# Kernel tuning notes

Measured on AMD Instinct MI355X. Metric: run time of the kernel, lower is better.

Reference implementation:

```python
import jax, jax.numpy as jnp
import numpy as np

B, S, D, H = 2, 4096, 512, 8
DK = D // H  # 64


def setup_inputs() -> dict:
    key = jax.random.key(0)
    ks = jax.random.split(key, 7)
    scale = 1.0 / np.sqrt(D)
    return {
        "query": jax.random.normal(ks[0], (B, S, D), dtype=jnp.float32),
        "key": jax.random.normal(ks[1], (B, S, D), dtype=jnp.float32),
        "value": jax.random.normal(ks[2], (B, S, D), dtype=jnp.float32),
        # nn.Linear weights, stored [out, in] as in torch; y = x @ W.T
        "Wq": jax.random.normal(ks[3], (D, D), dtype=jnp.float32) * scale,
        "Wk": jax.random.normal(ks[4], (D, D), dtype=jnp.float32) * scale,
        "Wv": jax.random.normal(ks[5], (D, D), dtype=jnp.float32) * scale,
        "Wo": jax.random.normal(ks[6], (D, D), dtype=jnp.float32) * scale,
    }


def reference(query, key, value, Wq, Wk, Wv, Wo):
    # projections (torch Linear: x @ W.T)
    q = query @ Wq.T  # [B,S,D]
    k = key @ Wk.T
    v = value @ Wv.T
    # split heads -> [B,H,S,DK]
    q = q.reshape(B, S, H, DK).transpose(0, 2, 1, 3)
    k = k.reshape(B, S, H, DK).transpose(0, 2, 1, 3)
    v = v.reshape(B, S, H, DK).transpose(0, 2, 1, 3)
    # scores [B,H,S,S], softmax, weighted sum (dropout=0 / eval)
    scores = jnp.einsum("bhqd,bhkd->bhqk", q, k) / np.sqrt(DK).astype(np.float32)
    weights = jax.nn.softmax(scores, axis=-1)
    attn = jnp.einsum("bhqk,bhkd->bhqd", weights, v)  # [B,H,S,DK]
    # merge heads -> [B,S,D], output projection
    out = attn.transpose(0, 2, 1, 3).reshape(B, S, D)
    return out @ Wo.T
```

## Files before the change

### kernel.cpp

```cpp
#include <hip/hip_runtime.h>
#include <hip/hip_bf16.h>

typedef short short8 __attribute__((ext_vector_type(8)));
typedef short short4v __attribute__((ext_vector_type(4)));
typedef float floatx4 __attribute__((ext_vector_type(4)));
typedef unsigned int uint4v __attribute__((ext_vector_type(4)));

constexpr int Bc = 2, Sc = 4096, Dc = 512, Hc = 8, DKc = 64;
constexpr int Mc = Bc * Sc;

static __device__ __forceinline__ unsigned short f2bf(float f) {
  unsigned int u = __builtin_bit_cast(unsigned int, f);
  unsigned int rb = ((u >> 16) & 1u) + 0x7fffu;
  return (unsigned short)((u + rb) >> 16);
}
static __device__ __forceinline__ unsigned int cvt_pk_bf16(float lo, float hi) {
  unsigned int r;
  asm("v_cvt_pk_bf16_f32 %0, %1, %2" : "=v"(r) : "v"(lo), "v"(hi));
  return r;
}
static __device__ __forceinline__ float exp2_fast(float x) {
  float r;
  asm("v_exp_f32 %0, %1" : "=v"(r) : "v"(x));
  return r;
}

__global__ __launch_bounds__(256) void cast_w(
    const float* __restrict__ a, const float* __restrict__ b,
    const float* __restrict__ c, const float* __restrict__ d,
    unsigned short* __restrict__ out) {
  const float* srcs[4] = {a, b, c, d};
  const int m = blockIdx.y;
  const int i = (blockIdx.x * 256 + threadIdx.x) * 4;
  float4 v = *(const float4*)(srcs[m] + i);
  unsigned short t4[4] = {f2bf(v.x), f2bf(v.y), f2bf(v.z), f2bf(v.w)};
  *(short4v*)(out + (size_t)m * (Dc * Dc) + i) = *(short4v*)t4;
}

template <int IN_F32, int OUT_F32>
__global__ __launch_bounds__(256) void gemm_bt(
    const void* __restrict__ Xv, const unsigned short* __restrict__ Wb,
    void* __restrict__ Yv, int Mdim, int N, int K) {
  constexpr int BM = 128, BN = 64, BK = 32, LDP = 40;
  __shared__ unsigned short As[BM * LDP];
  __shared__ unsigned short Bs[BN * LDP];
  const int tid = threadIdx.x;
  const int lane = tid & 63, wid = tid >> 6;
  const int wm = wid >> 1, wn = wid & 1;
  const int bm = blockIdx.y * BM, bn = blockIdx.x * BN;
  const int rq = lane & 15, kk8 = (lane >> 4) * 8;
  const int sr = tid >> 1, sc = (tid & 1) * 16;
  const int brow = tid >> 2, bc8 = (tid & 3) * 8;

  floatx4 acc[4][2] = {};

  for (int k0 = 0; k0 < K; k0 += BK) {
    if (IN_F32) {
      const float* src = (const float*)Xv + (size_t)(bm + sr) * K + k0 + sc;
      unsigned int t2[8];
#pragma unroll
      for (int i = 0; i < 4; ++i) {
        float4 v = *(const float4*)(src + i * 4);
        t2[i * 2 + 0] = cvt_pk_bf16(v.x, v.y);
        t2[i * 2 + 1] = cvt_pk_bf16(v.z, v.w);
      }
      uint4v u0 = {t2[0], t2[1], t2[2], t2[3]};
      uint4v u1 = {t2[4], t2[5], t2[6], t2[7]};
      *(uint4v*)&As[sr * LDP + sc] = u0;
      *(uint4v*)&As[sr * LDP + sc + 8] = u1;
    } else {
      const unsigned short* src =
          (const unsigned short*)Xv + (size_t)(bm + sr) * K + k0 + sc;
      *(short8*)&As[sr * LDP + sc] = *(const short8*)src;
      *(short8*)&As[sr * LDP + sc + 8] = *(const short8*)(src + 8);
    }
    *(short8*)&Bs[brow * LDP + bc8] =
        *(const short8*)(Wb + (size_t)(bn + brow) * K + k0 + bc8);
    __syncthreads();

    short8 af[4], bfr[2];
#pragma unroll
    for (int mi = 0; mi < 4; ++mi)
      af[mi] = *(const short8*)&As[(wm * 64 + mi * 16 + rq) * LDP + kk8];
#pragma unroll
    for (int ni = 0; ni < 2; ++ni)
      bfr[ni] = *(const short8*)&Bs[(wn * 32 + ni * 16 + rq) * LDP + kk8];
#pragma unroll
    for (int mi = 0; mi < 4; ++mi)
#pragma unroll
      for (int ni = 0; ni < 2; ++ni)
        acc[mi][ni] = __builtin_amdgcn_mfma_f32_16x16x32_bf16(
            af[mi], bfr[ni], acc[mi][ni], 0, 0, 0);
    __syncthreads();
  }

#pragma unroll
  for (int mi = 0; mi < 4; ++mi)
#pragma unroll
    for (int ni = 0; ni < 2; ++ni)
#pragma unroll
      for (int j = 0; j < 4; ++j) {
        int r = bm + wm * 64 + mi * 16 + (lane >> 4) * 4 + j;
        int c = bn + wn * 32 + ni * 16 + rq;
        float v = acc[mi][ni][j];
        if (OUT_F32)
          ((float*)Yv)[(size_t)r * N + c] = v;
        else
          ((unsigned short*)Yv)[(size_t)r * N + c] = f2bf(v);
      }
}

__global__ __launch_bounds__(256) void transpose_v(
    const unsigned short* __restrict__ vb, unsigned short* __restrict__ vt) {
  constexpr int LDT = 65;
  __shared__ unsigned short T[64 * LDT];
  const int tid = threadIdx.x;
  const int s0 = blockIdx.x * 64, c0 = blockIdx.y * 64, b = blockIdx.z;
  const int r = tid >> 2, cs = (tid & 3) * 16;
  const unsigned short* src = vb + ((size_t)b * Sc + s0 + r) * Dc + c0 + cs;
  *(short8*)&T[r * LDT + cs] = *(const short8*)src;
  *(short8*)&T[r * LDT + cs + 8] = *(const short8*)(src + 8);
  __syncthreads();
  unsigned short tmp[16];
#pragma unroll
  for (int j = 0; j < 16; ++j) tmp[j] = T[(cs + j) * LDT + r];
  const int k4 = (cs >> 4) & 1;
  const int base32 = s0 + (cs & 32);
  unsigned short* dstrow = vt + ((size_t)b * Dc + c0 + r) * Sc;
#pragma unroll
  for (int g = 0; g < 4; ++g) {
    short4v v4 = {(short)tmp[4 * g + 0], (short)tmp[4 * g + 1],
                  (short)tmp[4 * g + 2], (short)tmp[4 * g + 3]};
    *(short4v*)(dstrow + base32 + g * 8 + k4 * 4) = v4;
  }
}

__global__ __launch_bounds__(512, 4) void attn_fwd(
    const unsigned short* __restrict__ Qp, const unsigned short* __restrict__ Kp,
    const unsigned short* __restrict__ Vtp, unsigned short* __restrict__ Op) {
  __shared__ unsigned char smem[33792];
  unsigned short* KsB = (unsigned short*)smem;
  unsigned short* VsB = (unsigned short*)(smem + 16384);

  const int tid = threadIdx.x, lane = tid & 63, wid = tid >> 6;
  const int qc = wid >> 1, kh = wid & 1;
  const int b = blockIdx.y >> 3, h = blockIdx.y & 7;
  const int q0 = blockIdx.x * 128 + qc * 32;
  const int rq = lane & 15, lg = lane >> 4, kk8 = lg * 8;

  const unsigned short* Qb = Qp + ((size_t)b * Sc) * Dc + h * DKc;
  const unsigned short* Kb = Kp + ((size_t)b * Sc) * Dc + h * DKc;
  const unsigned short* Vh = Vtp + ((size_t)b * Dc + h * DKc) * Sc;

  short8 qa[2][2];
#pragma unroll
  for (int qi = 0; qi < 2; ++qi)
#pragma unroll
    for (int c = 0; c < 2; ++c)
      qa[qi][c] = *(const short8*)(Qb + (size_t)(q0 + qi * 16 + rq) * Dc + c * 32 + kk8);

  floatx4 o_acc[2][4] = {};
  float l_part[2] = {0.f, 0.f};
  float m_run[2] = {-1e30f, -1e30f};

  const float C2 = 0.18033688f;
  const float THR = 8.0f;

  const int sr = tid >> 3, sc8 = (tid & 7) * 8;
  const int st = (sr * 64 + sc8) ^ ((sr & 7) << 3);
  const int sx = (rq & 7) << 3;

  short8 kr = *(const short8*)(Kb + (size_t)sr * Dc + sc8);
  short8 vr = *(const short8*)(Vh + (size_t)sr * Sc + sc8);
  *(short8*)&KsB[st] = kr;
  *(short8*)&VsB[st] = vr;

  for (int it = 0; it < 64; ++it) {
    const int cur = it & 1;
    __syncthreads();

    if (it < 63) {
      const int kn = (it + 1) * 64;
      kr = *(const short8*)(Kb + (size_t)(kn + sr) * Dc + sc8);
      vr = *(const short8*)(Vh + (size_t)sr * Sc + kn + sc8);
    }

    const unsigned short* Ks = KsB + cur * 4096;
    const unsigned short* Vs = VsB + cur * 4096;

    short8 ka[2][2];
#pragma unroll
    for (int ks = 0; ks < 2; ++ks)
#pragma unroll
      for (int c = 0; c < 2; ++c) {
        const int row = kh * 32 + ks * 16 + rq;
        ka[ks][c] = *(const short8*)&Ks[(row * 64 + c * 32 + kk8) ^ sx];
      }

    short8 pb_[2];
#pragma unroll
    for (int qi = 0; qi < 2; ++qi) {
      floatx4 s[2] = {};
#pragma unroll
      for (int ks = 0; ks < 2; ++ks) {
        s[ks] = __builtin_amdgcn_mfma_f32_16x16x32_bf16(ka[ks][0], qa[qi][0], s[ks], 0, 0, 0);
        s[ks] = __builtin_amdgcn_mfma_f32_16x16x32_bf16(ka[ks][1], qa[qi][1], s[ks], 0, 0, 0);
      }
      float tp = fmaxf(fmaxf(fmaxf(s[0][0], s[0][1]), fmaxf(s[0][2], s[0][3])),
                       fmaxf(fmaxf(s[1][0], s[1][1]), fmaxf(s[1][2], s[1][3]))) * C2;

      if (__any(tp > m_run[qi] + THR)) {
        float tm = tp;
        tm = fmaxf(tm, __shfl_xor(tm, 16, 64));
        tm = fmaxf(tm, __shfl_xor(tm, 32, 64));
        if (__any(tm > m_run[qi])) {
          float mn = fmaxf(m_run[qi], tm);
          float scf = exp2_fast(m_run[qi] - mn);
          m_run[qi] = mn;
          l_part[qi] *= scf;
          float sc_c[4];
#pragma unroll
          for (int j = 0; j < 4; ++j) sc_c[j] = __shfl(scf, lg * 4 + j, 64);
#pragma unroll
          for (int j = 0; j < 4; ++j)
#pragma unroll
            for (int dt = 0; dt < 4; ++dt) o_acc[qi][dt][j] *= sc_c[j];
        }
      }

      const float lm = m_run[qi];
      unsigned int pw0, pw1, pw2, pw3;
      {
        float p0 = exp2_fast(fmaf(s[0][0], C2, -lm));
        float p1 = exp2_fast(fmaf(s[0][1], C2, -lm));
        float p2 = exp2_fast(fmaf(s[0][2], C2, -lm));
        float p3 = exp2_fast(fmaf(s[0][3], C2, -lm));
        l_part[qi] += (p0 + p1) + (p2 + p3);
        pw0 = cvt_pk_bf16(p0, p1);
        pw1 = cvt_pk_bf16(p2, p3);
      }
      {
        float p0 = exp2_fast(fmaf(s[1][0], C2, -lm));
        float p1 = exp2_fast(fmaf(s[1][1], C2, -lm));
        float p2 = exp2_fast(fmaf(s[1][2], C2, -lm));
        float p3 = exp2_fast(fmaf(s[1][3], C2, -lm));
        l_part[qi] += (p0 + p1) + (p2 + p3);
        pw2 = cvt_pk_bf16(p0, p1);
        pw3 = cvt_pk_bf16(p2, p3);
      }
      uint4v pw = {pw0, pw1, pw2, pw3};
      pb_[qi] = __builtin_bit_cast(short8, pw);
    }

#pragma unroll
    for (int dt = 0; dt < 4; ++dt) {
      const int vrow = dt * 16 + rq;
      short8 v = *(const short8*)&Vs[(vrow * 64 + kh * 32 + kk8) ^ sx];
      o_acc[0][dt] = __builtin_amdgcn_mfma_f32_16x16x32_bf16(pb_[0], v, o_acc[0][dt], 0, 0, 0);
      o_acc[1][dt] = __builtin_amdgcn_mfma_f32_16x16x32_bf16(pb_[1], v, o_acc[1][dt], 0, 0, 0);
    }

    if (it < 63) {
      *(short8*)&KsB[(cur ^ 1) * 4096 + st] = kr;
      *(short8*)&VsB[(cur ^ 1) * 4096 + st] = vr;
    }
  }

  float l_run[2];
#pragma unroll
  for (int qi = 0; qi < 2; ++qi) {
    float ls = l_part[qi];
    ls += __shfl_xor(ls, 16, 64);
    ls += __shfl_xor(ls, 32, 64);
    l_run[qi] = ls;
  }

  __syncthreads();
  float* MO = (float*)smem;
  float* ML = (float*)(smem + 32768);
  if (kh == 1) {
#pragma unroll
    for (int qi = 0; qi < 2; ++qi) {
#pragma unroll
      for (int j = 0; j < 4; ++j) {
        int row = qc * 32 + qi * 16 + lg * 4 + j;
#pragma unroll
        for (int dt = 0; dt < 4; ++dt)
          MO[(size_t)row * 64 + dt * 16 + rq] = o_acc[qi][dt][j];
      }
      if (lg == 0) {
        int row = qc * 32 + qi * 16 + rq;
        ML[row * 2 + 0] = m_run[qi];
        ML[row * 2 + 1] = l_run[qi];
      }
    }
  }
  __syncthreads();
  if (kh == 0) {
#pragma unroll
    for (int qi = 0; qi < 2; ++qi) {
      float m0c[4], l0c[4];
#pragma unroll
      for (int j = 0; j < 4; ++j) {
        m0c[j] = __shfl(m_run[qi], lg * 4 + j, 64);
        l0c[j] = __shfl(l_run[qi], lg * 4 + j, 64);
      }
#pragma unroll
      for (int j = 0; j < 4; ++j) {
        int row = qc * 32 + qi * 16 + lg * 4 + j;
        int r = q0 + qi * 16 + lg * 4 + j;
        float m1 = ML[row * 2 + 0], l1 = ML[row * 2 + 1];
        float mx = fmaxf(m0c[j], m1);
        float a0 = exp2_fast(m0c[j] - mx), a1 = exp2_fast(m1 - mx);
        float inv = 1.0f / (l0c[j] * a0 + l1 * a1);
#pragma unroll
        for (int dt = 0; dt < 4; ++dt) {
          float o = (o_acc[qi][dt][j] * a0 + MO[(size_t)row * 64 + dt * 16 + rq] * a1) * inv;
          Op[((size_t)b * Sc + r) * Dc + h * DKc + dt * 16 + rq] = f2bf(o);
        }
      }
    }
  }
}

extern "C" void kernel_launch(void* const* d_in, const int* in_sizes, int n_in,
                              void* d_out, int out_size, void* d_ws, size_t ws_size,
                              hipStream_t stream) {
  const float* q_in = (const float*)d_in[0];
  const float* k_in = (const float*)d_in[1];
  const float* v_in = (const float*)d_in[2];
  const float* Wq = (const float*)d_in[3];
  const float* Wk = (const float*)d_in[4];
  const float* Wv = (const float*)d_in[5];
  const float* Wo = (const float*)d_in[6];

  unsigned short* wq_b = (unsigned short*)d_ws;
  unsigned short* wk_b = wq_b + Dc * Dc;
  unsigned short* wv_b = wk_b + Dc * Dc;
  unsigned short* wo_b = wv_b + Dc * Dc;
  unsigned short* qb = wo_b + Dc * Dc;
  unsigned short* kb = qb + (size_t)Mc * Dc;
  unsigned short* vb = kb + (size_t)Mc * Dc;
  unsigned short* ab = vb + (size_t)Mc * Dc;
  unsigned short* vt = ab + (size_t)Mc * Dc;

  dim3 cg(Dc * Dc / 4 / 256, 4);
  cast_w<<<cg, 256, 0, stream>>>(Wq, Wk, Wv, Wo, wq_b);

  dim3 gg(Dc / 64, Mc / 128);
  gemm_bt<1, 0><<<gg, 256, 0, stream>>>(q_in, wq_b, qb, Mc, Dc, Dc);
  gemm_bt<1, 0><<<gg, 256, 0, stream>>>(k_in, wk_b, kb, Mc, Dc, Dc);
  gemm_bt<1, 0><<<gg, 256, 0, stream>>>(v_in, wv_b, vb, Mc, Dc, Dc);

  dim3 tg(Sc / 64, Dc / 64, Bc);
  transpose_v<<<tg, 256, 0, stream>>>(vb, vt);

  dim3 ga(Sc / 128, Bc * Hc);
  attn_fwd<<<ga, 512, 0, stream>>>(qb, kb, vt, ab);

  gemm_bt<0, 1><<<gg, 256, 0, stream>>>(ab, wo_b, (float*)d_out, Mc, Dc, Dc);
}
```

Baseline: 181.1 us.

## Fuse QKV projections, drop weight cast kernel, double-buffer GEMM LDS tiles

Removes the separate fp32-to-bf16 weight cast kernel by converting weights inside the GEMM tile load. The three Q/K/V projection GEMMs become a single launch using grid z to pick operands. The GEMM body now double-buffers LDS with register prefetch of the next K tile, so it needs only one barrier per iteration. This saves launch overhead and hides global load latency, at the cost of doubled LDS, more registers and redundant weight conversion in every block.

New measurement: 174.5 us. 1.04x faster.

```diff
diff --git a/kernel.cpp b/kernel.cpp
--- a/kernel.cpp
+++ b/kernel.cpp
@@ -25,25 +25,13 @@
   return r;
 }
 
-__global__ __launch_bounds__(256) void cast_w(
-    const float* __restrict__ a, const float* __restrict__ b,
-    const float* __restrict__ c, const float* __restrict__ d,
-    unsigned short* __restrict__ out) {
-  const float* srcs[4] = {a, b, c, d};
-  const int m = blockIdx.y;
-  const int i = (blockIdx.x * 256 + threadIdx.x) * 4;
-  float4 v = *(const float4*)(srcs[m] + i);
-  unsigned short t4[4] = {f2bf(v.x), f2bf(v.y), f2bf(v.z), f2bf(v.w)};
-  *(short4v*)(out + (size_t)m * (Dc * Dc) + i) = *(short4v*)t4;
-}
-
-template <int IN_F32, int OUT_F32>
-__global__ __launch_bounds__(256) void gemm_bt(
-    const void* __restrict__ Xv, const unsigned short* __restrict__ Wb,
-    void* __restrict__ Yv, int Mdim, int N, int K) {
+template <int IN_F32, int OUT_F32, int W_F32>
+static __device__ __forceinline__ void gemm_body(
+    const void* __restrict__ Xv, const void* __restrict__ Wp,
+    void* __restrict__ Yv, const int N, const int K) {
   constexpr int BM = 128, BN = 64, BK = 32, LDP = 40;
-  __shared__ unsigned short As[BM * LDP];
-  __shared__ unsigned short Bs[BN * LDP];
+  __shared__ unsigned short As[2][BM * LDP];
+  __shared__ unsigned short Bs[2][BN * LDP];
   const int tid = threadIdx.x;
   const int lane = tid & 63, wid = tid >> 6;
   const int wm = wid >> 1, wn = wid & 1;
@@ -54,44 +42,88 @@
 
   floatx4 acc[4][2] = {};
 
-  for (int k0 = 0; k0 < K; k0 += BK) {
+  float a32[16];
+  short8 a16[2];
+  float b32[8];
+  short8 b16;
+
+  auto load_tile = [&](int k0) {
     if (IN_F32) {
       const float* src = (const float*)Xv + (size_t)(bm + sr) * K + k0 + sc;
-      unsigned int t2[8];
 #pragma unroll
       for (int i = 0; i < 4; ++i) {
         float4 v = *(const float4*)(src + i * 4);
-        t2[i * 2 + 0] = cvt_pk_bf16(v.x, v.y);
-        t2[i * 2 + 1] = cvt_pk_bf16(v.z, v.w);
-      }
-      uint4v u0 = {t2[0], t2[1], t2[2], t2[3]};
-      uint4v u1 = {t2[4], t2[5], t2[6], t2[7]};
-      *(uint4v*)&As[sr * LDP + sc] = u0;
-      *(uint4v*)&As[sr * LDP + sc + 8] = u1;
+        a32[4 * i + 0] = v.x; a32[4 * i + 1] = v.y;
+        a32[4 * i + 2] = v.z; a32[4 * i + 3] = v.w;
+      }
     } else {
       const unsigned short* src =
           (const unsigned short*)Xv + (size_t)(bm + sr) * K + k0 + sc;
-      *(short8*)&As[sr * LDP + sc] = *(const short8*)src;
-      *(short8*)&As[sr * LDP + sc + 8] = *(const short8*)(src + 8);
-    }
-    *(short8*)&Bs[brow * LDP + bc8] =
-        *(const short8*)(Wb + (size_t)(bn + brow) * K + k0 + bc8);
+      a16[0] = *(const short8*)src;
+      a16[1] = *(const short8*)(src + 8);
+    }
+    if (W_F32) {
+      const float* wsrc = (const float*)Wp + (size_t)(bn + brow) * K + k0 + bc8;
+#pragma unroll
+      for (int i = 0; i < 2; ++i) {
+        float4 v = *(const float4*)(wsrc + i * 4);
+        b32[4 * i + 0] = v.x; b32[4 * i + 1] = v.y;
+        b32[4 * i + 2] = v.z; b32[4 * i + 3] = v.w;
+      }
+    } else {
+      b16 = *(const short8*)((const unsigned short*)Wp +
+                             (size_t)(bn + brow) * K + k0 + bc8);
+    }
+  };
+  auto store_tile = [&](int bf) {
+    if (IN_F32) {
+      unsigned int t2[8];
+#pragma unroll
+      for (int i = 0; i < 8; ++i) t2[i] = cvt_pk_bf16(a32[2 * i], a32[2 * i + 1]);
+      uint4v u0 = {t2[0], t2[1], t2[2], t2[3]};
+      uint4v u1 = {t2[4], t2[5], t2[6], t2[7]};
+      *(uint4v*)&As[bf][sr * LDP + sc] = u0;
+      *(uint4v*)&As[bf][sr * LDP + sc + 8] = u1;
+    } else {
+      *(short8*)&As[bf][sr * LDP + sc] = a16[0];
+      *(short8*)&As[bf][sr * LDP + sc + 8] = a16[1];
+    }
+    if (W_F32) {
+      unsigned int t2[4];
+#pragma unroll
+      for (int i = 0; i < 4; ++i) t2[i] = cvt_pk_bf16(b32[2 * i], b32[2 * i + 1]);
+      uint4v u = {t2[0], t2[1], t2[2], t2[3]};
+      *(uint4v*)&Bs[bf][brow * LDP + bc8] = u;
+    } else {
+      *(short8*)&Bs[bf][brow * LDP + bc8] = b16;
+    }
+  };
+
+  load_tile(0);
+  store_tile(0);
+
+  const int NK = K / BK;
+  for (int it = 0; it < NK; ++it) {
+    const int cur = it & 1;
     __syncthreads();
 
+    if (it < NK - 1) load_tile((it + 1) * BK);
+
     short8 af[4], bfr[2];
 #pragma unroll
     for (int mi = 0; mi < 4; ++mi)
-      af[mi] = *(const short8*)&As[(wm * 64 + mi * 16 + rq) * LDP + kk8];
+      af[mi] = *(const short8*)&As[cur][(wm * 64 + mi * 16 + rq) * LDP + kk8];
 #pragma unroll
     for (int ni = 0; ni < 2; ++ni)
-      bfr[ni] = *(const short8*)&Bs[(wn * 32 + ni * 16 + rq) * LDP + kk8];
+      bfr[ni] = *(const short8*)&Bs[cur][(wn * 32 + ni * 16 + rq) * LDP + kk8];
 #pragma unroll
     for (int mi = 0; mi < 4; ++mi)
 #pragma unroll
       for (int ni = 0; ni < 2; ++ni)
         acc[mi][ni] = __builtin_amdgcn_mfma_f32_16x16x32_bf16(
             af[mi], bfr[ni], acc[mi][ni], 0, 0, 0);
-    __syncthreads();
+
+    if (it < NK - 1) store_tile(cur ^ 1);
   }
 
 #pragma unroll
@@ -108,6 +140,25 @@
         else
           ((unsigned short*)Yv)[(size_t)r * N + c] = f2bf(v);
       }
+}
+
+__global__ __launch_bounds__(256) void gemm_qkv(
+    const float* __restrict__ xq, const float* __restrict__ xk,
+    const float* __restrict__ xv, const float* __restrict__ wq,
+    const float* __restrict__ wk, const float* __restrict__ wv,
+    unsigned short* __restrict__ yq, unsigned short* __restrict__ yk,
+    unsigned short* __restrict__ yv) {
+  const int z = blockIdx.z;
+  const float* X = (z == 0) ? xq : (z == 1) ? xk : xv;
+  const float* W = (z == 0) ? wq : (z == 1) ? wk : wv;
+  unsigned short* Y = (z == 0) ? yq : (z == 1) ? yk : yv;
+  gemm_body<1, 0, 1>(X, W, Y, Dc, Dc);
+}
+
+__global__ __launch_bounds__(256) void gemm_out(
+    const unsigned short* __restrict__ x, const float* __restrict__ w,
+    float* __restrict__ y) {
+  gemm_body<0, 1, 1>(x, w, y, Dc, Dc);
 }
 
 __global__ __launch_bounds__(256) void transpose_v(
@@ -334,23 +385,14 @@
   const float* Wv = (const float*)d_in[5];
   const float* Wo = (const float*)d_in[6];
 
-  unsigned short* wq_b = (unsigned short*)d_ws;
-  unsigned short* wk_b = wq_b + Dc * Dc;
-  unsigned short* wv_b = wk_b + Dc * Dc;
-  unsigned short* wo_b = wv_b + Dc * Dc;
-  unsigned short* qb = wo_b + Dc * Dc;
+  unsigned short* qb = (unsigned short*)d_ws;
   unsigned short* kb = qb + (size_t)Mc * Dc;
   unsigned short* vb = kb + (size_t)Mc * Dc;
   unsigned short* ab = vb + (size_t)Mc * Dc;
   unsigned short* vt = ab + (size_t)Mc * Dc;
 
-  dim3 cg(Dc * Dc / 4 / 256, 4);
-  cast_w<<<cg, 256, 0, stream>>>(Wq, Wk, Wv, Wo, wq_b);
-
-  dim3 gg(Dc / 64, Mc / 128);
-  gemm_bt<1, 0><<<gg, 256, 0, stream>>>(q_in, wq_b, qb, Mc, Dc, Dc);
-  gemm_bt<1, 0><<<gg, 256, 0, stream>>>(k_in, wk_b, kb, Mc, Dc, Dc);
-  gemm_bt<1, 0><<<gg, 256, 0, stream>>>(v_in, wv_b, vb, Mc, Dc, Dc);
+  dim3 gq(Dc / 64, Mc / 128, 3);
+  gemm_qkv<<<gq, 256, 0, stream>>>(q_in, k_in, v_in, Wq, Wk, Wv, qb, kb, vb);
 
   dim3 tg(Sc / 64, Dc / 64, Bc);
   transpose_v<<<tg, 256, 0, stream>>>(vb, vt);
@@ -358,5 +400,6 @@
   dim3 ga(Sc / 128, Bc * Hc);
   attn_fwd<<<ga, 512, 0, stream>>>(qb, kb, vt, ab);
 
-  gemm_bt<0, 1><<<gg, 256, 0, stream>>>(ab, wo_b, (float*)d_out, Mc, Dc, Dc);
-}
+  dim3 gg(Dc / 64, Mc / 128);
+  gemm_out<<<gg, 256, 0, stream>>>(ab, Wo, (float*)d_out);
+}
```
